# Kernel optimization log

Measured on AMD Instinct MI355X. Metric: run time of the kernel, lower is better.

## Reference

```python
import jax, jax.numpy as jnp
import numpy as np

LAYERS = 30
LAYERS_PER_STACK = 10  # layers // stacks
UP_SCALES = (10, 8)


def setup_inputs() -> dict:
    key = jax.random.key(0)
    ks = jax.random.split(key, 12)
    B, T_c, C_in = 4, 400, 80
    T = T_c * UP_SCALES[0] * UP_SCALES[1]  # 32000
    OUT_CH, RES_CH, GATE_CH, SKIP_CH = 256, 64, 128, 64
    s = 0.05  # small init scale to keep gates unsaturated
    inp = {
        "x": jax.random.randint(ks[0], (B, T), 0, OUT_CH, dtype=jnp.int64),
        "c": jax.random.normal(ks[1], (B, C_in, T_c), dtype=jnp.float32),
        "first_w": jax.random.normal(ks[2], (RES_CH, OUT_CH), dtype=jnp.float32) * s,
        "first_b": jnp.zeros((RES_CH,), dtype=jnp.float32),
        "dconv_w": jax.random.normal(ks[3], (LAYERS, GATE_CH, RES_CH, 2), dtype=jnp.float32) * s,
        "dconv_b": jnp.zeros((LAYERS, GATE_CH), dtype=jnp.float32),
        "cond_w": jax.random.normal(ks[4], (LAYERS, GATE_CH, C_in), dtype=jnp.float32) * s,
        "skip_w": jax.random.normal(ks[5], (LAYERS, SKIP_CH, GATE_CH // 2), dtype=jnp.float32) * s,
        "skip_b": jnp.zeros((LAYERS, SKIP_CH), dtype=jnp.float32),
        "out_w": jax.random.normal(ks[6], (LAYERS, RES_CH, GATE_CH // 2), dtype=jnp.float32) * s,
        "out_b": jnp.zeros((LAYERS, RES_CH), dtype=jnp.float32),
        "last_w1": jax.random.normal(ks[7], (SKIP_CH, SKIP_CH), dtype=jnp.float32) * s,
        "last_b1": jnp.zeros((SKIP_CH,), dtype=jnp.float32),
        "last_w2": jax.random.normal(ks[8], (OUT_CH, SKIP_CH), dtype=jnp.float32) * s,
        "last_b2": jnp.zeros((OUT_CH,), dtype=jnp.float32),
        "conv_in_w": jax.random.normal(ks[9], (C_in, C_in), dtype=jnp.float32) * s,
        "up_w0": jnp.full((2 * UP_SCALES[0] + 1,), 1.0 / (2 * UP_SCALES[0] + 1), dtype=jnp.float32),
        "up_w1": jnp.full((2 * UP_SCALES[1] + 1,), 1.0 / (2 * UP_SCALES[1] + 1), dtype=jnp.float32),
    }
    return inp


def _upsample(c, conv_in_w, up_ws):
    # conv_in: 1x1 (aux_context_window=0)
    c = jnp.einsum('oc,bct->bot', conv_in_w, c)
    for w, scale in zip(up_ws, UP_SCALES):
        c = jnp.repeat(c, scale, axis=-1)  # nearest-neighbor upsample along time
        B, C, T = c.shape
        k = w.shape[0]
        c = jax.lax.conv_general_dilated(
            c.reshape(B * C, 1, T), w.reshape(1, 1, k),
            window_strides=(1,), padding=[(scale, scale)],
        ).reshape(B, C, T)
    return c


def reference(x, c, first_w, first_b, dconv_w, dconv_b, cond_w, skip_w, skip_b,
              out_w, out_b, last_w1, last_b1, last_w2, last_b2, conv_in_w, up_w0, up_w1):
    B, T = x.shape
    c_up = _upsample(c, conv_in_w, (up_w0, up_w1))  # (B, 80, T)
    # first_conv on one-hot(x): gather columns of first_w -> (B, 64, T)
    h = first_w.T[x].transpose(0, 2, 1) + first_b[None, :, None]
    skips = jnp.zeros_like(h[:, :1, :1])  # broadcastable accumulator
    skips = 0.0
    for l in range(LAYERS):
        d = 2 ** (l % LAYERS_PER_STACK)
        # causal dilated conv, kernel_size=2: y[t] = W0 @ h[t-d] + W1 @ h[t]
        h_prev = jnp.pad(h, ((0, 0), (0, 0), (d, 0)))[:, :, :T]
        y = (jnp.einsum('oc,bct->bot', dconv_w[l, :, :, 0], h_prev)
             + jnp.einsum('oc,bct->bot', dconv_w[l, :, :, 1], h)
             + dconv_b[l][None, :, None]
             + jnp.einsum('oc,bct->bot', cond_w[l], c_up))
        a, g = jnp.split(y, 2, axis=1)
        z = jnp.tanh(a) * jax.nn.sigmoid(g)  # gated activation, (B, 64, T)
        skips = skips + jnp.einsum('oc,bct->bot', skip_w[l], z) + skip_b[l][None, :, None]
        h = jnp.einsum('oc,bct->bot', out_w[l], z) + out_b[l][None, :, None] + h
    out = jax.nn.relu(skips)
    out = jnp.einsum('oc,bct->bot', last_w1, out) + last_b1[None, :, None]
    out = jax.nn.relu(out)
    out = jnp.einsum('oc,bct->bot', last_w2, out) + last_b2[None, :, None]
    return out  # (B, 256, T) logits
```

## Files before the change

### kernel.cpp

```cpp
#include <hip/hip_runtime.h>

#define TF 32000

typedef short s8v __attribute__((ext_vector_type(8)));
typedef float f4v __attribute__((ext_vector_type(4)));
typedef unsigned int ui4 __attribute__((ext_vector_type(4)));

__device__ __forceinline__ float us2f(unsigned int u16) {
  union { float f; unsigned int i; } v; v.i = u16 << 16; return v.f;
}
__device__ __forceinline__ unsigned short f2b(float f) {
  union { float f; unsigned int u; } v; v.f = f;
  unsigned int u = v.u;
  u = (u + 0x7fffu + ((u >> 16) & 1u)) >> 16;
  return (unsigned short)u;
}
__device__ __forceinline__ float gatef(float a, float g) {
  a = fminf(fmaxf(a, -15.f), 15.f);
  float ta = __expf(2.f * a);
  float sg = __expf(-g);
  return (ta - 1.f) * __builtin_amdgcn_rcpf((ta + 1.f) * (1.f + sg));
}

__global__ void k_probe_x(const int* __restrict__ x, int* __restrict__ flag) {
  int acc = 0;
  for (int i = blockIdx.x * 256 + threadIdx.x; i < 64000; i += 32 * 256)
    acc |= x[2 * i + 1];
  unsigned long long m = __ballot(acc != 0);
  if ((threadIdx.x & 63) == 0 && m != 0ULL) atomicOr(flag, 1);
}

__global__ void k_probe_dt(const unsigned short* __restrict__ fw, int* __restrict__ flag) {
  int i = blockIdx.x * 256 + threadIdx.x;
  float v = us2f(fw[i]);
  int bad = !(fabsf(v) <= 1.0f);
  unsigned long long m = __ballot(bad);
  if ((threadIdx.x & 63) == 0 && m != 0ULL) atomicOr(flag, 2);
}

struct SrcPtrs { const void* p[17]; };

__global__ __launch_bounds__(256) void k_cvt(SrcPtrs sp, const int* __restrict__ flag,
                                             float* __restrict__ wdst, float* __restrict__ cdst) {
  int i = blockIdx.x * 256 + threadIdx.x;
  if (i >= 1223846) return;
  const bool f32 = ((*flag) & 2) != 0;
  int s, base;
  if (i < 507968) {
    if (i < 16384)       { s = 0;  base = 0; }
    else if (i < 16448)  { s = 1;  base = 16384; }
    else                 { s = 2;  base = 16448; }
  } else if (i < 943808) {
    if (i < 511808)      { s = 3;  base = 507968; }
    else if (i < 819008) { s = 4;  base = 511808; }
    else if (i < 941888) { s = 5;  base = 819008; }
    else                 { s = 6;  base = 941888; }
  } else if (i < 1089408) {
    if (i < 1066688)      { s = 7;  base = 943808; }
    else if (i < 1068608) { s = 8;  base = 1066688; }
    else if (i < 1072704) { s = 9;  base = 1068608; }
    else if (i < 1072768) { s = 10; base = 1072704; }
    else if (i < 1089152) { s = 11; base = 1072768; }
    else                  { s = 12; base = 1089152; }
  } else {
    if (i < 1095808)      { s = 13; base = 1089408; }
    else if (i < 1095829) { s = 14; base = 1095808; }
    else if (i < 1095846) { s = 15; base = 1095829; }
    else                  { s = 16; base = 1095846; }
  }
  int j = i - base;
  const void* src = sp.p[s];
  float v = f32 ? ((const float*)src)[j] : us2f(((const unsigned short*)src)[j]);
  if (s == 16) cdst[j] = v; else wdst[i] = v;
}

__global__ __launch_bounds__(256) void k_pack(const float* __restrict__ wc,
    unsigned short* __restrict__ w1h, unsigned short* __restrict__ w1l,
    unsigned short* __restrict__ w2h, unsigned short* __restrict__ w2l) {
  int i = blockIdx.x * 256 + threadIdx.x;
  if (i < 860160) {
    int l = i / 28672, r = i % 28672, o = r / 224, k = r % 224;
    float v = 0.f;
    if (k < 128)      v = wc[16448 + l * 16384 + o * 128 + (k & 63) * 2 + (k >> 6)];
    else if (k < 208) v = wc[511808 + l * 10240 + o * 80 + (k - 128)];
    unsigned short hh = f2b(v);
    w1h[i] = hh;
    w1l[i] = f2b(v - us2f(hh));
  } else if (i < 1105920) {
    int j = i - 860160;
    int l = j / 8192, r = j % 8192, o = r / 64, ch = r % 64;
    float v = (o < 64) ? wc[819008 + l * 4096 + o * 64 + ch]
                       : wc[943808 + l * 4096 + (o - 64) * 64 + ch];
    unsigned short hh = f2b(v);
    w2h[j] = hh;
    w2l[j] = f2b(v - us2f(hh));
  }
}

__global__ void k_convin(const float* __restrict__ c, const float* __restrict__ w,
                         float* __restrict__ c0) {
  int b = blockIdx.x / 400, t = blockIdx.x % 400;
  int o = threadIdx.x;
  if (o >= 80) return;
  const float* crow = c + b * 80 * 400 + t;
  const float* wrow = w + o * 80;
  float acc = 0.f;
  for (int k = 0; k < 80; ++k) acc += wrow[k] * crow[k * 400];
  c0[(b * 80 + o) * 400 + t] = acc;
}

__global__ void k_up1(const float* __restrict__ c0, const float* __restrict__ w,
                      float* __restrict__ s1) {
  int id = blockIdx.x * 256 + threadIdx.x;
  int t = id % 4000;
  int bc = id / 4000;
  const float* src = c0 + bc * 400;
  float acc = 0.f;
  #pragma unroll
  for (int j = 0; j < 21; ++j) {
    int tt = t - 10 + j;
    if (tt >= 0 && tt < 4000) acc += w[j] * src[tt / 10];
  }
  s1[id] = acc;
}

__global__ void k_up2(const float* __restrict__ s1, const float* __restrict__ w,
                      unsigned int* __restrict__ cpk) {
  int id = blockIdx.x * 256 + threadIdx.x;
  int t = id % TF;
  int cp = (id / TF) % 40;
  int b = id / (40 * TF);
  const float* src0 = s1 + (b * 80 + cp * 2) * 4000;
  const float* src1 = src0 + 4000;
  float a0 = 0.f, a1 = 0.f;
  #pragma unroll
  for (int j = 0; j < 17; ++j) {
    int tt = t - 8 + j;
    if (tt >= 0 && tt < TF) {
      int q = tt / 8;
      a0 += w[j] * src0[q];
      a1 += w[j] * src1[q];
    }
  }
  cpk[id] = (unsigned int)f2b(a0) | ((unsigned int)f2b(a1) << 16);
}

__global__ void k_first(const int* __restrict__ x, const int* __restrict__ flag,
                        const float* __restrict__ fw, const float* __restrict__ fb,
                        unsigned int* __restrict__ hhi, unsigned int* __restrict__ hlo) {
  int id = blockIdx.x * 256 + threadIdx.x;
  int t = id % TF;
  int rp = (id / TF) & 31;
  int b = id / (32 * TF);
  int i = b * TF + t;
  int idx = (((*flag) & 1) ? x[i] : x[2 * i]) & 255;
  int r0 = rp * 2;
  float v0 = fw[r0 * 256 + idx] + fb[r0];
  float v1 = fw[(r0 + 1) * 256 + idx] + fb[r0 + 1];
  unsigned int h0 = f2b(v0), h1 = f2b(v1);
  hhi[id] = h0 | (h1 << 16);
  hlo[id] = (unsigned int)f2b(v0 - us2f(h0)) | ((unsigned int)f2b(v1 - us2f(h1)) << 16);
}

__global__ __launch_bounds__(256, 4) void k_layer(
    const unsigned int* __restrict__ hhi_in, const unsigned int* __restrict__ hlo_in,
    unsigned int* __restrict__ hhi_out, unsigned int* __restrict__ hlo_out,
    float* __restrict__ skips, const unsigned int* __restrict__ cpk,
    const unsigned short* __restrict__ w1h, const unsigned short* __restrict__ w1l,
    const unsigned short* __restrict__ w2h, const unsigned short* __restrict__ w2l,
    const float* __restrict__ db, const float* __restrict__ sb,
    const float* __restrict__ ob, int d, int mode) {
  __shared__ __align__(16) unsigned char smem[34816];
  unsigned short (*Xhi)[136] = (unsigned short (*)[136])smem;
  unsigned short (*Xlo)[136] = (unsigned short (*)[136])(smem + 17408);
  unsigned short (*Zhi)[72]  = (unsigned short (*)[72])smem;
  unsigned short (*Zlo)[72]  = (unsigned short (*)[72])(smem + 9216);
  const int obid = (blockIdx.x & 7) * 250 + (blockIdx.x >> 3);
  const int b = obid / 500;
  const int t0 = (obid % 500) * 64;
  const int tid = threadIdx.x;
  const int wv = tid >> 6, l15 = tid & 15, kl = (tid >> 4) & 3;
  const int R0 = wv * 16, R1 = 64 + wv * 16;
  const int ko = kl * 8;
  const unsigned int* hhiB = hhi_in + (size_t)b * 32 * TF;
  const unsigned int* hloB = hlo_in + (size_t)b * 32 * TF;
  const unsigned int* cpkB = cpk + (size_t)b * 40 * TF;

  const int r0e = R0 + kl * 4;
  float* sp_ = skips + ((size_t)b * 64 + r0e) * TF + t0;
  float s_old[16];
  if (!(mode & 1)) {
    #pragma unroll
    for (int ct = 0; ct < 4; ++ct) {
      const int t = ct * 16 + l15;
      s_old[ct * 4 + 0] = sp_[0 * TF + t];
      s_old[ct * 4 + 1] = sp_[1 * TF + t];
      s_old[ct * 4 + 2] = sp_[2 * TF + t];
      s_old[ct * 4 + 3] = sp_[3 * TF + t];
    }
  } else {
    #pragma unroll
    for (int q = 0; q < 16; ++q) s_old[q] = 0.f;
  }

  const bool d4 = (d & 3) == 0;
  for (int u = tid; u < 1024; u += 256) {
    const int g = u & 63, blk = u >> 6;
    const int cp = (g & 7) | ((blk & 3) << 3);
    const int tq = (g >> 3) | ((blk & 4) << 1);
    const int arr = blk >> 3;
    const int row = cp * TF;
    ui4 hv, lv;
    if (arr == 0) {
      hv = *(const ui4*)(hhiB + row + t0 + tq * 4);
      lv = *(const ui4*)(hloB + row + t0 + tq * 4);
    } else {
      const int base = t0 - d + tq * 4;
      if (d4 && base >= 0) {
        hv = *(const ui4*)(hhiB + row + base);
        lv = *(const ui4*)(hloB + row + base);
      } else {
        #pragma unroll
        for (int q = 0; q < 4; ++q) {
          int tp = base + q;
          hv[q] = tp >= 0 ? hhiB[row + tp] : 0u;
          lv[q] = tp >= 0 ? hloB[row + tp] : 0u;
        }
      }
    }
    const int colb = (arr ? 0 : 64) + cp * 2;
    #pragma unroll
    for (int q = 0; q < 4; ++q) {
      const int t = tq * 4 + q;
      *(unsigned int*)&Xhi[t][colb] = hv[q];
      *(unsigned int*)&Xlo[t][colb] = lv[q];
    }
  }
  __syncthreads();

  f4v accA[4], accG[4];
  {
    f4v bA = *(const f4v*)(db + R0 + kl * 4);
    f4v bG = *(const f4v*)(db + R1 + kl * 4);
    #pragma unroll
    for (int ct = 0; ct < 4; ++ct) { accA[ct] = bA; accG[ct] = bG; }
  }
  #pragma unroll
  for (int s = 0; s < 4; ++s) {
    const int k0 = s * 32 + ko;
    s8v ah0 = *(const s8v*)(w1h + (R0 + l15) * 224 + k0);
    s8v ah1 = *(const s8v*)(w1h + (R1 + l15) * 224 + k0);
    s8v al0 = *(const s8v*)(w1l + (R0 + l15) * 224 + k0);
    s8v al1 = *(const s8v*)(w1l + (R1 + l15) * 224 + k0);
    #pragma unroll
    for (int ct = 0; ct < 4; ++ct) {
      s8v bh = *(const s8v*)&Xhi[ct * 16 + l15][k0];
      s8v bl = *(const s8v*)&Xlo[ct * 16 + l15][k0];
      accA[ct] = __builtin_amdgcn_mfma_f32_16x16x32_bf16(ah0, bh, accA[ct], 0, 0, 0);
      accG[ct] = __builtin_amdgcn_mfma_f32_16x16x32_bf16(ah1, bh, accG[ct], 0, 0, 0);
      accA[ct] = __builtin_amdgcn_mfma_f32_16x16x32_bf16(al0, bh, accA[ct], 0, 0, 0);
      accG[ct] = __builtin_amdgcn_mfma_f32_16x16x32_bf16(al1, bh, accG[ct], 0, 0, 0);
      accA[ct] = __builtin_amdgcn_mfma_f32_16x16x32_bf16(ah0, bl, accA[ct], 0, 0, 0);
      accG[ct] = __builtin_amdgcn_mfma_f32_16x16x32_bf16(ah1, bl, accG[ct], 0, 0, 0);
    }
  }
  #pragma unroll
  for (int s = 4; s < 7; ++s) {
    const int k0 = s * 32 + ko;
    s8v ah0 = *(const s8v*)(w1h + (R0 + l15) * 224 + k0);
    s8v ah1 = *(const s8v*)(w1h + (R1 + l15) * 224 + k0);
    s8v al0 = *(const s8v*)(w1l + (R0 + l15) * 224 + k0);
    s8v al1 = *(const s8v*)(w1l + (R1 + l15) * 224 + k0);
    const int cp0 = (k0 - 128) >> 1;
    #pragma unroll
    for (int ct = 0; ct < 4; ++ct) {
      const int tg = t0 + ct * 16 + l15;
      ui4 cv;
      #pragma unroll
      for (int m = 0; m < 4; ++m)
        cv[m] = (cp0 + m < 40) ? cpkB[(cp0 + m) * TF + tg] : 0u;
      s8v bh = __builtin_bit_cast(s8v, cv);
      accA[ct] = __builtin_amdgcn_mfma_f32_16x16x32_bf16(ah0, bh, accA[ct], 0, 0, 0);
      accG[ct] = __builtin_amdgcn_mfma_f32_16x16x32_bf16(ah1, bh, accG[ct], 0, 0, 0);
      accA[ct] = __builtin_amdgcn_mfma_f32_16x16x32_bf16(al0, bh, accA[ct], 0, 0, 0);
      accG[ct] = __builtin_amdgcn_mfma_f32_16x16x32_bf16(al1, bh, accG[ct], 0, 0, 0);
    }
  }

  float rres[16];
  #pragma unroll
  for (int ct = 0; ct < 4; ++ct) {
    const int t = ct * 16 + l15;
    uint2 rh = *(const uint2*)&Xhi[t][64 + R0 + kl * 4];
    uint2 rl = *(const uint2*)&Xlo[t][64 + R0 + kl * 4];
    rres[ct * 4 + 0] = us2f(rh.x & 0xffffu) + us2f(rl.x & 0xffffu);
    rres[ct * 4 + 1] = us2f(rh.x >> 16)     + us2f(rl.x >> 16);
    rres[ct * 4 + 2] = us2f(rh.y & 0xffffu) + us2f(rl.y & 0xffffu);
    rres[ct * 4 + 3] = us2f(rh.y >> 16)     + us2f(rl.y >> 16);
  }
  __syncthreads();

  #pragma unroll
  for (int ct = 0; ct < 4; ++ct) {
    const int t = ct * 16 + l15;
    unsigned int hw[2], lw[2];
    #pragma unroll
    for (int p = 0; p < 2; ++p) {
      float z0 = gatef(accA[ct][2 * p],     accG[ct][2 * p]);
      float z1 = gatef(accA[ct][2 * p + 1], accG[ct][2 * p + 1]);
      unsigned int h0 = f2b(z0), h1 = f2b(z1);
      hw[p] = h0 | (h1 << 16);
      lw[p] = (unsigned int)f2b(z0 - us2f(h0)) | ((unsigned int)f2b(z1 - us2f(h1)) << 16);
    }
    uint2 hv; hv.x = hw[0]; hv.y = hw[1];
    uint2 lv; lv.x = lw[0]; lv.y = lw[1];
    *(uint2*)&Zhi[t][R0 + kl * 4] = hv;
    *(uint2*)&Zlo[t][R0 + kl * 4] = lv;
  }
  __syncthreads();

  f4v accS[4], accH[4];
  {
    f4v bS = *(const f4v*)(sb + R0 + kl * 4);
    f4v bO = *(const f4v*)(ob + R0 + kl * 4);
    #pragma unroll
    for (int ct = 0; ct < 4; ++ct) { accS[ct] = bS; accH[ct] = bO; }
  }
  #pragma unroll
  for (int s = 0; s < 2; ++s) {
    const int k0 = s * 32 + ko;
    s8v ah0 = *(const s8v*)(w2h + (R0 + l15) * 64 + k0);
    s8v ah1 = *(const s8v*)(w2h + (R1 + l15) * 64 + k0);
    s8v al0 = *(const s8v*)(w2l + (R0 + l15) * 64 + k0);
    s8v al1 = *(const s8v*)(w2l + (R1 + l15) * 64 + k0);
    #pragma unroll
    for (int ct = 0; ct < 4; ++ct) {
      s8v bh = *(const s8v*)&Zhi[ct * 16 + l15][k0];
      s8v bl = *(const s8v*)&Zlo[ct * 16 + l15][k0];
      accS[ct] = __builtin_amdgcn_mfma_f32_16x16x32_bf16(ah0, bh, accS[ct], 0, 0, 0);
      accH[ct] = __builtin_amdgcn_mfma_f32_16x16x32_bf16(ah1, bh, accH[ct], 0, 0, 0);
      accS[ct] = __builtin_amdgcn_mfma_f32_16x16x32_bf16(al0, bh, accS[ct], 0, 0, 0);
      accH[ct] = __builtin_amdgcn_mfma_f32_16x16x32_bf16(al1, bh, accH[ct], 0, 0, 0);
      accS[ct] = __builtin_amdgcn_mfma_f32_16x16x32_bf16(ah0, bl, accS[ct], 0, 0, 0);
      accH[ct] = __builtin_amdgcn_mfma_f32_16x16x32_bf16(ah1, bl, accH[ct], 0, 0, 0);
    }
  }

  unsigned int* hho = hhi_out + ((size_t)b * 32 + (r0e >> 1)) * TF + t0;
  unsigned int* hlo = hlo_out + ((size_t)b * 32 + (r0e >> 1)) * TF + t0;
  #pragma unroll
  for (int ct = 0; ct < 4; ++ct) {
    const int t = ct * 16 + l15;
    sp_[0 * TF + t] = s_old[ct * 4 + 0] + accS[ct][0];
    sp_[1 * TF + t] = s_old[ct * 4 + 1] + accS[ct][1];
    sp_[2 * TF + t] = s_old[ct * 4 + 2] + accS[ct][2];
    sp_[3 * TF + t] = s_old[ct * 4 + 3] + accS[ct][3];
    if (!(mode & 2)) {
      float h0 = accH[ct][0] + rres[ct * 4 + 0];
      float h1 = accH[ct][1] + rres[ct * 4 + 1];
      float h2 = accH[ct][2] + rres[ct * 4 + 2];
      float h3 = accH[ct][3] + rres[ct * 4 + 3];
      unsigned int a0 = f2b(h0), a1 = f2b(h1), a2 = f2b(h2), a3 = f2b(h3);
      hho[t]      = a0 | (a1 << 16);
      hho[TF + t] = a2 | (a3 << 16);
      hlo[t]      = (unsigned int)f2b(h0 - us2f(a0)) | ((unsigned int)f2b(h1 - us2f(a1)) << 16);
      hlo[TF + t] = (unsigned int)f2b(h2 - us2f(a2)) | ((unsigned int)f2b(h3 - us2f(a3)) << 16);
    }
  }
}

__global__ __launch_bounds__(256, 4) void k_final(
    const float* __restrict__ skips,
    const float* __restrict__ w1, const float* __restrict__ b1,
    const float* __restrict__ w2, const float* __restrict__ b2,
    float* __restrict__ out) {
  __shared__ __align__(16) unsigned short Shi[64][72];
  __shared__ __align__(16) unsigned short Slo[64][72];
  __shared__ __align__(16) unsigned short Zhi[64][72];
  __shared__ __align__(16) unsigned short Zlo[64][72];
  const int obid = (blockIdx.x & 7) * 250 + (blockIdx.x >> 3);
  const int b = obid / 500;
  const int t0 = (obid % 500) * 64;
  const int tid = threadIdx.x;
  const float* sbase = skips + (size_t)b * 64 * TF;

  for (int u = tid; u < 512; u += 256) {
    const int cp = u >> 4, tq = u & 15, ch0 = cp * 2;
    float4 A = *(const float4*)(sbase + (size_t)ch0 * TF + t0 + tq * 4);
    float4 B = *(const float4*)(sbase + (size_t)(ch0 + 1) * TF + t0 + tq * 4);
    float va[4] = {fmaxf(A.x, 0.f), fmaxf(A.y, 0.f), fmaxf(A.z, 0.f), fmaxf(A.w, 0.f)};
    float vb[4] = {fmaxf(B.x, 0.f), fmaxf(B.y, 0.f), fmaxf(B.z, 0.f), fmaxf(B.w, 0.f)};
    #pragma unroll
    for (int j = 0; j < 4; ++j) {
      int t = tq * 4 + j;
      unsigned int h0 = f2b(va[j]), h1 = f2b(vb[j]);
      *(unsigned int*)&Shi[t][ch0] = h0 | (h1 << 16);
      *(unsigned int*)&Slo[t][ch0] =
          (unsigned int)f2b(va[j] - us2f(h0)) | ((unsigned int)f2b(vb[j] - us2f(h1)) << 16);
    }
  }
  __syncthreads();

  const int wv = tid >> 6, l15 = tid & 15, kl = (tid >> 4) & 3;
  const int R = wv * 16;

  f4v acc[4];
  {
    f4v bb = *(const f4v*)(b1 + R + kl * 4);
    #pragma unroll
    for (int ct = 0; ct < 4; ++ct) acc[ct] = bb;
  }
  #pragma unroll
  for (int ks = 0; ks < 2; ++ks) {
    const int k0 = ks * 32 + kl * 8;
    const float* wr = w1 + (R + l15) * 64 + k0;
    s8v ah, al;
    #pragma unroll
    for (int m = 0; m < 8; ++m) {
      float v = wr[m];
      unsigned short hh = f2b(v);
      ah[m] = (short)hh;
      al[m] = (short)f2b(v - us2f(hh));
    }
    #pragma unroll
    for (int ct = 0; ct < 4; ++ct) {
      s8v bh = *(const s8v*)&Shi[ct * 16 + l15][k0];
      s8v bl = *(const s8v*)&Slo[ct * 16 + l15][k0];
      acc[ct] = __builtin_amdgcn_mfma_f32_16x16x32_bf16(ah, bh, acc[ct], 0, 0, 0);
      acc[ct] = __builtin_amdgcn_mfma_f32_16x16x32_bf16(al, bh, acc[ct], 0, 0, 0);
      acc[ct] = __builtin_amdgcn_mfma_f32_16x16x32_bf16(ah, bl, acc[ct], 0, 0, 0);
    }
  }
  #pragma unroll
  for (int ct = 0; ct < 4; ++ct) {
    const int t = ct * 16 + l15;
    unsigned int hw[2], lw[2];
    #pragma unroll
    for (int p = 0; p < 2; ++p) {
      float z0 = fmaxf(acc[ct][2 * p], 0.f);
      float z1 = fmaxf(acc[ct][2 * p + 1], 0.f);
      unsigned int h0 = f2b(z0), h1 = f2b(z1);
      hw[p] = h0 | (h1 << 16);
      lw[p] = (unsigned int)f2b(z0 - us2f(h0)) | ((unsigned int)f2b(z1 - us2f(h1)) << 16);
    }
    uint2 hv; hv.x = hw[0]; hv.y = hw[1];
    uint2 lv; lv.x = lw[0]; lv.y = lw[1];
    *(uint2*)&Zhi[t][R + kl * 4] = hv;
    *(uint2*)&Zlo[t][R + kl * 4] = lv;
  }
  __syncthreads();

  float* obase = out + (size_t)b * 256 * TF + t0;
  #pragma unroll
  for (int g = 0; g < 4; ++g) {
    const int R2 = g * 64 + wv * 16;
    f4v a2[4];
    {
      f4v bb = *(const f4v*)(b2 + R2 + kl * 4);
      #pragma unroll
      for (int ct = 0; ct < 4; ++ct) a2[ct] = bb;
    }
    #pragma unroll
    for (int ks = 0; ks < 2; ++ks) {
      const int k0 = ks * 32 + kl * 8;
      const float* wr = w2 + (R2 + l15) * 64 + k0;
      s8v ah, al;
      #pragma unroll
      for (int m = 0; m < 8; ++m) {
        float v = wr[m];
        unsigned short hh = f2b(v);
        ah[m] = (short)hh;
        al[m] = (short)f2b(v - us2f(hh));
      }
      #pragma unroll
      for (int ct = 0; ct < 4; ++ct) {
        s8v bh = *(const s8v*)&Zhi[ct * 16 + l15][k0];
        s8v bl = *(const s8v*)&Zlo[ct * 16 + l15][k0];
        a2[ct] = __builtin_amdgcn_mfma_f32_16x16x32_bf16(ah, bh, a2[ct], 0, 0, 0);
        a2[ct] = __builtin_amdgcn_mfma_f32_16x16x32_bf16(al, bh, a2[ct], 0, 0, 0);
        a2[ct] = __builtin_amdgcn_mfma_f32_16x16x32_bf16(ah, bl, a2[ct], 0, 0, 0);
      }
    }
    const int r0 = R2 + kl * 4;
    #pragma unroll
    for (int ct = 0; ct < 4; ++ct) {
      const int t = ct * 16 + l15;
      obase[(size_t)(r0 + 0) * TF + t] = a2[ct][0];
      obase[(size_t)(r0 + 1) * TF + t] = a2[ct][1];
      obase[(size_t)(r0 + 2) * TF + t] = a2[ct][2];
      obase[(size_t)(r0 + 3) * TF + t] = a2[ct][3];
    }
  }
}

extern "C" void kernel_launch(void* const* d_in, const int* in_sizes, int n_in,
                              void* d_out, int out_size, void* d_ws, size_t ws_size,
                              hipStream_t stream) {
  const int* x = (const int*)d_in[0];

  float* ws = (float*)d_ws;
  int*   flag = (int*)ws;
  float* wcan = ws + 16;
  unsigned int* cpkb = (unsigned int*)(ws + 1095872);
  float* ha    = ws + 6215872;
  float* hbuf  = ws + 14407872;
  float* skips = ws + 22599872;
  float* cin = ha;
  float* c0  = ha + 128000;
  float* s1f = ha + 256000;
  if (ws_size < (size_t)30791872 * 4) return;

  unsigned int* haHi = (unsigned int*)ha;
  unsigned int* haLo = haHi + 4096000;
  unsigned int* hbHi = (unsigned int*)hbuf;
  unsigned int* hbLo = hbHi + 4096000;

  float* fwc = wcan;            float* fbc = wcan + 16384;
  float* dbc = wcan + 507968;
  float* sbc = wcan + 941888;
  float* obc = wcan + 1066688;  float* w1c = wcan + 1068608;
  float* b1c = wcan + 1072704;  float* w2c = wcan + 1072768;
  float* b2c = wcan + 1089152;  float* ciwc = wcan + 1089408;
  float* uw0c = wcan + 1095808; float* uw1c = wcan + 1095829;

  unsigned short* wp = (unsigned short*)d_out;
  unsigned short* W1H = wp;
  unsigned short* W1L = wp + 860160;
  unsigned short* W2H = wp + 1720320;
  unsigned short* W2L = wp + 1966080;

  hipMemsetAsync(flag, 0, 64, stream);
  k_probe_x<<<dim3(32), dim3(256), 0, stream>>>(x, flag);
  k_probe_dt<<<dim3(64), dim3(256), 0, stream>>>((const unsigned short*)d_in[2], flag);

  SrcPtrs sp;
  sp.p[0] = d_in[2];  sp.p[1] = d_in[3];  sp.p[2] = d_in[4];  sp.p[3] = d_in[5];
  sp.p[4] = d_in[6];  sp.p[5] = d_in[7];  sp.p[6] = d_in[8];  sp.p[7] = d_in[9];
  sp.p[8] = d_in[10]; sp.p[9] = d_in[11]; sp.p[10] = d_in[12]; sp.p[11] = d_in[13];
  sp.p[12] = d_in[14]; sp.p[13] = d_in[15]; sp.p[14] = d_in[16]; sp.p[15] = d_in[17];
  sp.p[16] = d_in[1];
  k_cvt<<<dim3(4781), dim3(256), 0, stream>>>(sp, flag, wcan, cin);
  k_pack<<<dim3(4320), dim3(256), 0, stream>>>(wcan, W1H, W1L, W2H, W2L);

  k_convin<<<dim3(1600), dim3(128), 0, stream>>>(cin, ciwc, c0);
  k_up1<<<dim3(5000), dim3(256), 0, stream>>>(c0, uw0c, s1f);
  k_up2<<<dim3(20000), dim3(256), 0, stream>>>(s1f, uw1c, cpkb);
  k_first<<<dim3(16000), dim3(256), 0, stream>>>(x, flag, fwc, fbc, haHi, haLo);

  unsigned int* hiIn = haHi; unsigned int* loIn = haLo;
  unsigned int* hiOut = hbHi; unsigned int* loOut = hbLo;
  for (int l = 0; l < 30; ++l) {
    int d = 1 << (l % 10);
    int mode = (l == 0 ? 1 : 0) | (l == 29 ? 2 : 0);
    k_layer<<<dim3(2000), dim3(256), 0, stream>>>(
        hiIn, loIn, hiOut, loOut, skips, cpkb,
        W1H + (size_t)l * 28672, W1L + (size_t)l * 28672,
        W2H + (size_t)l * 8192,  W2L + (size_t)l * 8192,
        dbc + l * 128, sbc + l * 64, obc + l * 64, d, mode);
    unsigned int* t;
    t = hiIn; hiIn = hiOut; hiOut = t;
    t = loIn; loIn = loOut; loOut = t;
  }
  k_final<<<dim3(2000), dim3(256), 0, stream>>>(skips, w1c, b1c, w2c, b2c,
                                                (float*)d_out);
}
```

Before: 1.765 ms.

## Fuse pairs of small-dilation WaveNet layers into one kernel with halo recompute

Adds a templated k_fused kernel that computes two consecutive residual layers (dilations 1/2, 4/8, 16/32) per launch. The first layer is recomputed over a halo of extra time rows so the second layer's dilated input stays in shared memory. This removes the global write and read of h and one skips read-modify-write between the paired layers, and cuts launches from 30 to 21. In exchange it does redundant first-layer compute over the halo rows, uses more shared memory and registers, and lowers the occupancy hint to 3 blocks.

```diff
diff --git a/kernel.cpp b/kernel.cpp
--- a/kernel.cpp
+++ b/kernel.cpp
@@ -291,8 +291,8 @@
   #pragma unroll
   for (int ct = 0; ct < 4; ++ct) {
     const int t = ct * 16 + l15;
-    uint2 rh = *(const uint2*)&Xhi[t][64 + R0 + kl * 4];
-    uint2 rl = *(const uint2*)&Xlo[t][64 + R0 + kl * 4];
+    uint2 rh = *(const uint2*)&Xhi[t][64 + r0e];
+    uint2 rl = *(const uint2*)&Xlo[t][64 + r0e];
     rres[ct * 4 + 0] = us2f(rh.x & 0xffffu) + us2f(rl.x & 0xffffu);
     rres[ct * 4 + 1] = us2f(rh.x >> 16)     + us2f(rl.x >> 16);
     rres[ct * 4 + 2] = us2f(rh.y & 0xffffu) + us2f(rl.y & 0xffffu);
@@ -314,15 +314,15 @@
     }
     uint2 hv; hv.x = hw[0]; hv.y = hw[1];
     uint2 lv; lv.x = lw[0]; lv.y = lw[1];
-    *(uint2*)&Zhi[t][R0 + kl * 4] = hv;
-    *(uint2*)&Zlo[t][R0 + kl * 4] = lv;
+    *(uint2*)&Zhi[t][r0e] = hv;
+    *(uint2*)&Zlo[t][r0e] = lv;
   }
   __syncthreads();
 
   f4v accS[4], accH[4];
   {
-    f4v bS = *(const f4v*)(sb + R0 + kl * 4);
-    f4v bO = *(const f4v*)(ob + R0 + kl * 4);
+    f4v bS = *(const f4v*)(sb + r0e);
+    f4v bO = *(const f4v*)(ob + r0e);
     #pragma unroll
     for (int ct = 0; ct < 4; ++ct) { accS[ct] = bS; accH[ct] = bO; }
   }
@@ -366,6 +366,363 @@
       hlo[t]      = (unsigned int)f2b(h0 - us2f(a0)) | ((unsigned int)f2b(h1 - us2f(a1)) << 16);
       hlo[TF + t] = (unsigned int)f2b(h2 - us2f(a2)) | ((unsigned int)f2b(h3 - us2f(a3)) << 16);
     }
+  }
+}
+
+template<int ROWS>
+__global__ __launch_bounds__(256, 3) void k_fused(
+    const unsigned int* __restrict__ hhi_in, const unsigned int* __restrict__ hlo_in,
+    unsigned int* __restrict__ hhi_out, unsigned int* __restrict__ hlo_out,
+    float* __restrict__ skips, const unsigned int* __restrict__ cpk,
+    const unsigned short* __restrict__ w1hA, const unsigned short* __restrict__ w1lA,
+    const unsigned short* __restrict__ w2hA, const unsigned short* __restrict__ w2lA,
+    const float* __restrict__ dbA, const float* __restrict__ sbA, const float* __restrict__ obA,
+    const unsigned short* __restrict__ w1hB, const unsigned short* __restrict__ w1lB,
+    const unsigned short* __restrict__ w2hB, const unsigned short* __restrict__ w2lB,
+    const float* __restrict__ dbB, const float* __restrict__ sbB, const float* __restrict__ obB,
+    int d1, int d2, int mode) {
+  constexpr int HALO = ROWS - 64;
+  constexpr int CT1 = ROWS / 16;
+  constexpr int OG0 = HALO / 16;
+  constexpr int TQ = ROWS / 4;
+  __shared__ __align__(16) unsigned char smem[ROWS * 544];
+  typedef unsigned short (*a64)[64];
+  typedef unsigned short (*a72)[72];
+  a64 XpvH = (a64)(smem);
+  a64 XpvL = (a64)(smem + ROWS * 128);
+  a64 XcH  = (a64)(smem + ROWS * 256);
+  a64 XcL  = (a64)(smem + ROWS * 384);
+  a72 Z1H  = (a72)(smem);
+  a72 Z1L  = (a72)(smem + ROWS * 144);
+  a64 X2H  = (a64)(smem + ROWS * 288);
+  a64 X2L  = (a64)(smem + ROWS * 416);
+  a72 Z2H  = (a72)(smem);
+  a72 Z2L  = (a72)(smem + 9216);
+
+  const int obid = (blockIdx.x & 7) * 250 + (blockIdx.x >> 3);
+  const int b = obid / 500;
+  const int t0 = (obid % 500) * 64;
+  const int tb = t0 - HALO;
+  const int tid = threadIdx.x;
+  const int wv = tid >> 6, l15 = tid & 15, kl = (tid >> 4) & 3;
+  const int R0 = wv * 16, R1 = 64 + wv * 16;
+  const int ko = kl * 8;
+  const unsigned int* hhiB = hhi_in + (size_t)b * 32 * TF;
+  const unsigned int* hloB = hlo_in + (size_t)b * 32 * TF;
+  const unsigned int* cpkB = cpk + (size_t)b * 40 * TF;
+
+  const int r0e = R0 + kl * 4;
+  float* sp_ = skips + ((size_t)b * 64 + r0e) * TF + t0;
+  float s_old[16];
+  if (!(mode & 1)) {
+    #pragma unroll
+    for (int og = 0; og < 4; ++og) {
+      const int t = og * 16 + l15;
+      s_old[og * 4 + 0] = sp_[0 * TF + t];
+      s_old[og * 4 + 1] = sp_[1 * TF + t];
+      s_old[og * 4 + 2] = sp_[2 * TF + t];
+      s_old[og * 4 + 3] = sp_[3 * TF + t];
+    }
+  } else {
+    #pragma unroll
+    for (int q = 0; q < 16; ++q) s_old[q] = 0.f;
+  }
+
+  const bool d4 = (d1 & 3) == 0;
+  for (int u = tid; u < 2 * 32 * TQ; u += 256) {
+    const int tq = u % TQ;
+    const int cp = (u / TQ) & 31;
+    const int arr = u / (32 * TQ);
+    const int rowg = cp * TF;
+    const int base = tb + tq * 4 - (arr ? d1 : 0);
+    ui4 hv, lv;
+    if (base >= 0 && (arr == 0 || d4)) {
+      hv = *(const ui4*)(hhiB + rowg + base);
+      lv = *(const ui4*)(hloB + rowg + base);
+    } else {
+      #pragma unroll
+      for (int q = 0; q < 4; ++q) {
+        int tp = base + q;
+        hv[q] = tp >= 0 ? hhiB[rowg + tp] : 0u;
+        lv[q] = tp >= 0 ? hloB[rowg + tp] : 0u;
+      }
+    }
+    const int colb = cp * 2;
+    if (arr == 0) {
+      #pragma unroll
+      for (int q = 0; q < 4; ++q) {
+        *(unsigned int*)&XcH[tq * 4 + q][colb] = hv[q];
+        *(unsigned int*)&XcL[tq * 4 + q][colb] = lv[q];
+      }
+    } else {
+      #pragma unroll
+      for (int q = 0; q < 4; ++q) {
+        *(unsigned int*)&XpvH[tq * 4 + q][colb] = hv[q];
+        *(unsigned int*)&XpvL[tq * 4 + q][colb] = lv[q];
+      }
+    }
+  }
+  __syncthreads();
+
+  f4v accA[CT1], accG[CT1];
+  {
+    f4v bA = *(const f4v*)(dbA + r0e);
+    f4v bG = *(const f4v*)(dbA + R1 + kl * 4);
+    #pragma unroll
+    for (int g = 0; g < CT1; ++g) { accA[g] = bA; accG[g] = bG; }
+  }
+  #pragma unroll
+  for (int s = 0; s < 4; ++s) {
+    const int k0 = s * 32 + ko;
+    s8v ah0 = *(const s8v*)(w1hA + (R0 + l15) * 224 + k0);
+    s8v ah1 = *(const s8v*)(w1hA + (R1 + l15) * 224 + k0);
+    s8v al0 = *(const s8v*)(w1lA + (R0 + l15) * 224 + k0);
+    s8v al1 = *(const s8v*)(w1lA + (R1 + l15) * 224 + k0);
+    #pragma unroll
+    for (int g = 0; g < CT1; ++g) {
+      const int r = g * 16 + l15;
+      s8v bh, bl;
+      if (s < 2) { bh = *(const s8v*)&XpvH[r][k0];      bl = *(const s8v*)&XpvL[r][k0]; }
+      else       { bh = *(const s8v*)&XcH[r][k0 - 64];  bl = *(const s8v*)&XcL[r][k0 - 64]; }
+      accA[g] = __builtin_amdgcn_mfma_f32_16x16x32_bf16(ah0, bh, accA[g], 0, 0, 0);
+      accG[g] = __builtin_amdgcn_mfma_f32_16x16x32_bf16(ah1, bh, accG[g], 0, 0, 0);
+      accA[g] = __builtin_amdgcn_mfma_f32_16x16x32_bf16(al0, bh, accA[g], 0, 0, 0);
+      accG[g] = __builtin_amdgcn_mfma_f32_16x16x32_bf16(al1, bh, accG[g], 0, 0, 0);
+      accA[g] = __builtin_amdgcn_mfma_f32_16x16x32_bf16(ah0, bl, accA[g], 0, 0, 0);
+      accG[g] = __builtin_amdgcn_mfma_f32_16x16x32_bf16(ah1, bl, accG[g], 0, 0, 0);
+    }
+  }
+  #pragma unroll
+  for (int s = 4; s < 7; ++s) {
+    const int k0 = s * 32 + ko;
+    s8v ah0 = *(const s8v*)(w1hA + (R0 + l15) * 224 + k0);
+    s8v ah1 = *(const s8v*)(w1hA + (R1 + l15) * 224 + k0);
+    s8v al0 = *(const s8v*)(w1lA + (R0 + l15) * 224 + k0);
+    s8v al1 = *(const s8v*)(w1lA + (R1 + l15) * 224 + k0);
+    const int cp0 = (k0 - 128) >> 1;
+    #pragma unroll
+    for (int g = 0; g < CT1; ++g) {
+      const int tg = tb + g * 16 + l15;
+      ui4 cv;
+      #pragma unroll
+      for (int m = 0; m < 4; ++m)
+        cv[m] = (tg >= 0 && cp0 + m < 40) ? cpkB[(cp0 + m) * TF + tg] : 0u;
+      s8v bh = __builtin_bit_cast(s8v, cv);
+      accA[g] = __builtin_amdgcn_mfma_f32_16x16x32_bf16(ah0, bh, accA[g], 0, 0, 0);
+      accG[g] = __builtin_amdgcn_mfma_f32_16x16x32_bf16(ah1, bh, accG[g], 0, 0, 0);
+      accA[g] = __builtin_amdgcn_mfma_f32_16x16x32_bf16(al0, bh, accA[g], 0, 0, 0);
+      accG[g] = __builtin_amdgcn_mfma_f32_16x16x32_bf16(al1, bh, accG[g], 0, 0, 0);
+    }
+  }
+
+  float rres1[CT1 * 4];
+  #pragma unroll
+  for (int g = 0; g < CT1; ++g) {
+    const int r = g * 16 + l15;
+    uint2 rh = *(const uint2*)&XcH[r][r0e];
+    uint2 rl = *(const uint2*)&XcL[r][r0e];
+    rres1[g * 4 + 0] = us2f(rh.x & 0xffffu) + us2f(rl.x & 0xffffu);
+    rres1[g * 4 + 1] = us2f(rh.x >> 16)     + us2f(rl.x >> 16);
+    rres1[g * 4 + 2] = us2f(rh.y & 0xffffu) + us2f(rl.y & 0xffffu);
+    rres1[g * 4 + 3] = us2f(rh.y >> 16)     + us2f(rl.y >> 16);
+  }
+  __syncthreads();
+
+  #pragma unroll
+  for (int g = 0; g < CT1; ++g) {
+    const int r = g * 16 + l15;
+    unsigned int hw[2], lw[2];
+    #pragma unroll
+    for (int p = 0; p < 2; ++p) {
+      float z0 = gatef(accA[g][2 * p],     accG[g][2 * p]);
+      float z1 = gatef(accA[g][2 * p + 1], accG[g][2 * p + 1]);
+      unsigned int h0 = f2b(z0), h1 = f2b(z1);
+      hw[p] = h0 | (h1 << 16);
+      lw[p] = (unsigned int)f2b(z0 - us2f(h0)) | ((unsigned int)f2b(z1 - us2f(h1)) << 16);
+    }
+    uint2 hv; hv.x = hw[0]; hv.y = hw[1];
+    uint2 lv; lv.x = lw[0]; lv.y = lw[1];
+    *(uint2*)&Z1H[r][r0e] = hv;
+    *(uint2*)&Z1L[r][r0e] = lv;
+  }
+  __syncthreads();
+
+  f4v accS1[CT1], accH1[CT1];
+  {
+    f4v bS = *(const f4v*)(sbA + r0e);
+    f4v bO = *(const f4v*)(obA + r0e);
+    #pragma unroll
+    for (int g = 0; g < CT1; ++g) { accS1[g] = bS; accH1[g] = bO; }
+  }
+  #pragma unroll
+  for (int s = 0; s < 2; ++s) {
+    const int k0 = s * 32 + ko;
+    s8v ah0 = *(const s8v*)(w2hA + (R0 + l15) * 64 + k0);
+    s8v ah1 = *(const s8v*)(w2hA + (R1 + l15) * 64 + k0);
+    s8v al0 = *(const s8v*)(w2lA + (R0 + l15) * 64 + k0);
+    s8v al1 = *(const s8v*)(w2lA + (R1 + l15) * 64 + k0);
+    #pragma unroll
+    for (int g = 0; g < CT1; ++g) {
+      s8v bh = *(const s8v*)&Z1H[g * 16 + l15][k0];
+      s8v bl = *(const s8v*)&Z1L[g * 16 + l15][k0];
+      accS1[g] = __builtin_amdgcn_mfma_f32_16x16x32_bf16(ah0, bh, accS1[g], 0, 0, 0);
+      accH1[g] = __builtin_amdgcn_mfma_f32_16x16x32_bf16(ah1, bh, accH1[g], 0, 0, 0);
+      accS1[g] = __builtin_amdgcn_mfma_f32_16x16x32_bf16(al0, bh, accS1[g], 0, 0, 0);
+      accH1[g] = __builtin_amdgcn_mfma_f32_16x16x32_bf16(al1, bh, accH1[g], 0, 0, 0);
+      accS1[g] = __builtin_amdgcn_mfma_f32_16x16x32_bf16(ah0, bl, accS1[g], 0, 0, 0);
+      accH1[g] = __builtin_amdgcn_mfma_f32_16x16x32_bf16(ah1, bl, accH1[g], 0, 0, 0);
+    }
+  }
+  #pragma unroll
+  for (int g = 0; g < CT1; ++g) {
+    const int r = g * 16 + l15;
+    const int tg = tb + r;
+    float h0 = accH1[g][0] + rres1[g * 4 + 0];
+    float h1 = accH1[g][1] + rres1[g * 4 + 1];
+    float h2 = accH1[g][2] + rres1[g * 4 + 2];
+    float h3 = accH1[g][3] + rres1[g * 4 + 3];
+    if (tg < 0) { h0 = 0.f; h1 = 0.f; h2 = 0.f; h3 = 0.f; }
+    unsigned int a0 = f2b(h0), a1 = f2b(h1), a2 = f2b(h2), a3 = f2b(h3);
+    uint2 hv, lv;
+    hv.x = a0 | (a1 << 16);
+    hv.y = a2 | (a3 << 16);
+    lv.x = (unsigned int)f2b(h0 - us2f(a0)) | ((unsigned int)f2b(h1 - us2f(a1)) << 16);
+    lv.y = (unsigned int)f2b(h2 - us2f(a2)) | ((unsigned int)f2b(h3 - us2f(a3)) << 16);
+    *(uint2*)&X2H[r][r0e] = hv;
+    *(uint2*)&X2L[r][r0e] = lv;
+  }
+  f4v sOwn[4];
+  #pragma unroll
+  for (int og = 0; og < 4; ++og) sOwn[og] = accS1[og + OG0];
+  __syncthreads();
+
+  f4v accA2[4], accG2[4];
+  {
+    f4v bA = *(const f4v*)(dbB + r0e);
+    f4v bG = *(const f4v*)(dbB + R1 + kl * 4);
+    #pragma unroll
+    for (int og = 0; og < 4; ++og) { accA2[og] = bA; accG2[og] = bG; }
+  }
+  #pragma unroll
+  for (int s = 0; s < 4; ++s) {
+    const int k0 = s * 32 + ko;
+    s8v ah0 = *(const s8v*)(w1hB + (R0 + l15) * 224 + k0);
+    s8v ah1 = *(const s8v*)(w1hB + (R1 + l15) * 224 + k0);
+    s8v al0 = *(const s8v*)(w1lB + (R0 + l15) * 224 + k0);
+    s8v al1 = *(const s8v*)(w1lB + (R1 + l15) * 224 + k0);
+    #pragma unroll
+    for (int og = 0; og < 4; ++og) {
+      const int r = HALO + og * 16 + l15;
+      s8v bh, bl;
+      if (s < 2) { bh = *(const s8v*)&X2H[r - d2][k0];     bl = *(const s8v*)&X2L[r - d2][k0]; }
+      else       { bh = *(const s8v*)&X2H[r][k0 - 64];     bl = *(const s8v*)&X2L[r][k0 - 64]; }
+      accA2[og] = __builtin_amdgcn_mfma_f32_16x16x32_bf16(ah0, bh, accA2[og], 0, 0, 0);
+      accG2[og] = __builtin_amdgcn_mfma_f32_16x16x32_bf16(ah1, bh, accG2[og], 0, 0, 0);
+      accA2[og] = __builtin_amdgcn_mfma_f32_16x16x32_bf16(al0, bh, accA2[og], 0, 0, 0);
+      accG2[og] = __builtin_amdgcn_mfma_f32_16x16x32_bf16(al1, bh, accG2[og], 0, 0, 0);
+      accA2[og] = __builtin_amdgcn_mfma_f32_16x16x32_bf16(ah0, bl, accA2[og], 0, 0, 0);
+      accG2[og] = __builtin_amdgcn_mfma_f32_16x16x32_bf16(ah1, bl, accG2[og], 0, 0, 0);
+    }
+  }
+  #pragma unroll
+  for (int s = 4; s < 7; ++s) {
+    const int k0 = s * 32 + ko;
+    s8v ah0 = *(const s8v*)(w1hB + (R0 + l15) * 224 + k0);
+    s8v ah1 = *(const s8v*)(w1hB + (R1 + l15) * 224 + k0);
+    s8v al0 = *(const s8v*)(w1lB + (R0 + l15) * 224 + k0);
+    s8v al1 = *(const s8v*)(w1lB + (R1 + l15) * 224 + k0);
+    const int cp0 = (k0 - 128) >> 1;
+    #pragma unroll
+    for (int og = 0; og < 4; ++og) {
+      const int tg = t0 + og * 16 + l15;
+      ui4 cv;
+      #pragma unroll
+      for (int m = 0; m < 4; ++m)
+        cv[m] = (cp0 + m < 40) ? cpkB[(cp0 + m) * TF + tg] : 0u;
+      s8v bh = __builtin_bit_cast(s8v, cv);
+      accA2[og] = __builtin_amdgcn_mfma_f32_16x16x32_bf16(ah0, bh, accA2[og], 0, 0, 0);
+      accG2[og] = __builtin_amdgcn_mfma_f32_16x16x32_bf16(ah1, bh, accG2[og], 0, 0, 0);
+      accA2[og] = __builtin_amdgcn_mfma_f32_16x16x32_bf16(al0, bh, accA2[og], 0, 0, 0);
+      accG2[og] = __builtin_amdgcn_mfma_f32_16x16x32_bf16(al1, bh, accG2[og], 0, 0, 0);
+    }
+  }
+
+  float rres2[16];
+  #pragma unroll
+  for (int og = 0; og < 4; ++og) {
+    const int r = HALO + og * 16 + l15;
+    uint2 rh = *(const uint2*)&X2H[r][r0e];
+    uint2 rl = *(const uint2*)&X2L[r][r0e];
+    rres2[og * 4 + 0] = us2f(rh.x & 0xffffu) + us2f(rl.x & 0xffffu);
+    rres2[og * 4 + 1] = us2f(rh.x >> 16)     + us2f(rl.x >> 16);
+    rres2[og * 4 + 2] = us2f(rh.y & 0xffffu) + us2f(rl.y & 0xffffu);
+    rres2[og * 4 + 3] = us2f(rh.y >> 16)     + us2f(rl.y >> 16);
+  }
+
+  #pragma unroll
+  for (int og = 0; og < 4; ++og) {
+    const int r = og * 16 + l15;
+    unsigned int hw[2], lw[2];
+    #pragma unroll
+    for (int p = 0; p < 2; ++p) {
+      float z0 = gatef(accA2[og][2 * p],     accG2[og][2 * p]);
+      float z1 = gatef(accA2[og][2 * p + 1], accG2[og][2 * p + 1]);
+      unsigned int h0 = f2b(z0), h1 = f2b(z1);
+      hw[p] = h0 | (h1 << 16);
+      lw[p] = (unsigned int)f2b(z0 - us2f(h0)) | ((unsigned int)f2b(z1 - us2f(h1)) << 16);
+    }
+    uint2 hv; hv.x = hw[0]; hv.y = hw[1];
+    uint2 lv; lv.x = lw[0]; lv.y = lw[1];
+    *(uint2*)&Z2H[r][r0e] = hv;
+    *(uint2*)&Z2L[r][r0e] = lv;
+  }
+  __syncthreads();
+
+  f4v accS2[4], accH2[4];
+  {
+    f4v bS = *(const f4v*)(sbB + r0e);
+    f4v bO = *(const f4v*)(obB + r0e);
+    #pragma unroll
+    for (int og = 0; og < 4; ++og) { accS2[og] = bS; accH2[og] = bO; }
+  }
+  #pragma unroll
+  for (int s = 0; s < 2; ++s) {
+    const int k0 = s * 32 + ko;
+    s8v ah0 = *(const s8v*)(w2hB + (R0 + l15) * 64 + k0);
+    s8v ah1 = *(const s8v*)(w2hB + (R1 + l15) * 64 + k0);
+    s8v al0 = *(const s8v*)(w2lB + (R0 + l15) * 64 + k0);
+    s8v al1 = *(const s8v*)(w2lB + (R1 + l15) * 64 + k0);
+    #pragma unroll
+    for (int og = 0; og < 4; ++og) {
+      s8v bh = *(const s8v*)&Z2H[og * 16 + l15][k0];
+      s8v bl = *(const s8v*)&Z2L[og * 16 + l15][k0];
+      accS2[og] = __builtin_amdgcn_mfma_f32_16x16x32_bf16(ah0, bh, accS2[og], 0, 0, 0);
+      accH2[og] = __builtin_amdgcn_mfma_f32_16x16x32_bf16(ah1, bh, accH2[og], 0, 0, 0);
+      accS2[og] = __builtin_amdgcn_mfma_f32_16x16x32_bf16(al0, bh, accS2[og], 0, 0, 0);
+      accH2[og] = __builtin_amdgcn_mfma_f32_16x16x32_bf16(al1, bh, accH2[og], 0, 0, 0);
+      accS2[og] = __builtin_amdgcn_mfma_f32_16x16x32_bf16(ah0, bl, accS2[og], 0, 0, 0);
+      accH2[og] = __builtin_amdgcn_mfma_f32_16x16x32_bf16(ah1, bl, accH2[og], 0, 0, 0);
+    }
+  }
+
+  unsigned int* hho = hhi_out + ((size_t)b * 32 + (r0e >> 1)) * TF + t0;
+  unsigned int* hlo = hlo_out + ((size_t)b * 32 + (r0e >> 1)) * TF + t0;
+  #pragma unroll
+  for (int og = 0; og < 4; ++og) {
+    const int t = og * 16 + l15;
+    sp_[0 * TF + t] = s_old[og * 4 + 0] + sOwn[og][0] + accS2[og][0];
+    sp_[1 * TF + t] = s_old[og * 4 + 1] + sOwn[og][1] + accS2[og][1];
+    sp_[2 * TF + t] = s_old[og * 4 + 2] + sOwn[og][2] + accS2[og][2];
+    sp_[3 * TF + t] = s_old[og * 4 + 3] + sOwn[og][3] + accS2[og][3];
+    float h0 = accH2[og][0] + rres2[og * 4 + 0];
+    float h1 = accH2[og][1] + rres2[og * 4 + 1];
+    float h2 = accH2[og][2] + rres2[og * 4 + 2];
+    float h3 = accH2[og][3] + rres2[og * 4 + 3];
+    unsigned int a0 = f2b(h0), a1 = f2b(h1), a2 = f2b(h2), a3 = f2b(h3);
+    hho[t]      = a0 | (a1 << 16);
+    hho[TF + t] = a2 | (a3 << 16);
+    hlo[t]      = (unsigned int)f2b(h0 - us2f(a0)) | ((unsigned int)f2b(h1 - us2f(a1)) << 16);
+    hlo[TF + t] = (unsigned int)f2b(h2 - us2f(a2)) | ((unsigned int)f2b(h3 - us2f(a3)) << 16);
   }
 }
 
@@ -549,17 +906,37 @@
 
   unsigned int* hiIn = haHi; unsigned int* loIn = haLo;
   unsigned int* hiOut = hbHi; unsigned int* loOut = hbLo;
-  for (int l = 0; l < 30; ++l) {
-    int d = 1 << (l % 10);
-    int mode = (l == 0 ? 1 : 0) | (l == 29 ? 2 : 0);
-    k_layer<<<dim3(2000), dim3(256), 0, stream>>>(
-        hiIn, loIn, hiOut, loOut, skips, cpkb,
-        W1H + (size_t)l * 28672, W1L + (size_t)l * 28672,
-        W2H + (size_t)l * 8192,  W2L + (size_t)l * 8192,
-        dbc + l * 128, sbc + l * 64, obc + l * 64, d, mode);
-    unsigned int* t;
-    t = hiIn; hiIn = hiOut; hiOut = t;
-    t = loIn; loIn = loOut; loOut = t;
+  for (int l = 0; l < 30; ) {
+    int m10 = l % 10;
+    if (m10 == 0 || m10 == 2 || m10 == 4) {
+      int d1 = 1 << m10, d2 = 1 << (m10 + 1);
+      auto kern = (m10 == 4) ? &k_fused<96> : &k_fused<80>;
+      kern<<<dim3(2000), dim3(256), 0, stream>>>(
+          hiIn, loIn, hiOut, loOut, skips, cpkb,
+          W1H + (size_t)l * 28672, W1L + (size_t)l * 28672,
+          W2H + (size_t)l * 8192,  W2L + (size_t)l * 8192,
+          dbc + l * 128, sbc + l * 64, obc + l * 64,
+          W1H + (size_t)(l + 1) * 28672, W1L + (size_t)(l + 1) * 28672,
+          W2H + (size_t)(l + 1) * 8192,  W2L + (size_t)(l + 1) * 8192,
+          dbc + (l + 1) * 128, sbc + (l + 1) * 64, obc + (l + 1) * 64,
+          d1, d2, (l == 0 ? 1 : 0));
+      unsigned int* t;
+      t = hiIn; hiIn = hiOut; hiOut = t;
+      t = loIn; loIn = loOut; loOut = t;
+      l += 2;
+    } else {
+      int d = 1 << m10;
+      int mode = (l == 29 ? 2 : 0);
+      k_layer<<<dim3(2000), dim3(256), 0, stream>>>(
+          hiIn, loIn, hiOut, loOut, skips, cpkb,
+          W1H + (size_t)l * 28672, W1L + (size_t)l * 28672,
+          W2H + (size_t)l * 8192,  W2L + (size_t)l * 8192,
+          dbc + l * 128, sbc + l * 64, obc + l * 64, d, mode);
+      unsigned int* t;
+      t = hiIn; hiIn = hiOut; hiOut = t;
+      t = loIn; loIn = loOut; loOut = t;
+      l += 1;
+    }
   }
   k_final<<<dim3(2000), dim3(256), 0, stream>>>(skips, w1c, b1c, w2c, b2c,
                                                 (float*)d_out);
```

Result: slower. 1.963 ms (+11.2%).
